# Performance work log

Hardware: AMD Instinct MI355X
Metric: run time of the kernel (lower is better)

The kernel has to match this reference:

```python
import jax, jax.numpy as jnp
import numpy as np

B, L, D = 32, 2048, 1024


def setup_inputs() -> dict:
    key = jax.random.key(0)
    ks = jax.random.split(key, 8)
    s = 1.0 / np.sqrt(D).astype(np.float32)  # torch nn.Linear init scale
    return {
        "decoder_hidden": jax.random.normal(ks[0], (B, 1, D), jnp.float32),
        "encoder_outputs": jax.random.normal(ks[1], (B, L, D), jnp.float32),
        "W_w": jax.random.uniform(ks[2], (D, D), jnp.float32, -s, s),
        "W_b": jax.random.uniform(ks[3], (D,), jnp.float32, -s, s),
        "U_w": jax.random.uniform(ks[4], (D, D), jnp.float32, -s, s),
        "U_b": jax.random.uniform(ks[5], (D,), jnp.float32, -s, s),
        "v_w": jax.random.uniform(ks[6], (1, D), jnp.float32, -s, s),
        "v_b": jax.random.uniform(ks[7], (1,), jnp.float32, -s, s),
    }


def reference(decoder_hidden, encoder_outputs, W_w, W_b, U_w, U_b, v_w, v_b):
    # torch Linear: y = x @ W.T + b
    q = decoder_hidden @ W_w.T + W_b            # [B, 1, D]
    k = encoder_outputs @ U_w.T + U_b           # [B, L, D]
    scores = jnp.tanh(q + k) @ v_w.T + v_b      # [B, L, 1]
    attn = jax.nn.softmax(scores[..., 0], axis=-1)[:, None, :]  # [B, 1, L]
    context = jnp.einsum("bql,bld->bqd", attn, encoder_outputs)  # [B, 1, D]
    return (context, attn)
```

## Files before the change

### kernel.cpp

```cpp
#include <hip/hip_runtime.h>
#include <hip/hip_bf16.h>
#include <stdint.h>

#define BB 32
#define LL 2048
#define DD 1024

typedef short short8  __attribute__((ext_vector_type(8)));
typedef float f32x4   __attribute__((ext_vector_type(4)));

__device__ __forceinline__ short f2bf(float f) {
    unsigned u = __float_as_uint(f);
    u += 0x7fffu + ((u >> 16) & 1u);
    return (short)(u >> 16);
}

__device__ __forceinline__ float bf2f(unsigned short s) {
    return __uint_as_float(((unsigned)s) << 16);
}

__device__ __forceinline__ float fast_tanh(float x) {
    float e = __expf(2.f * x);
    return 1.f - 2.f * __builtin_amdgcn_rcpf(e + 1.f);
}

__device__ __forceinline__ void async_cp16(const void* g, void* l) {
    __builtin_amdgcn_global_load_lds(
        (__attribute__((address_space(1))) void*)g,
        (__attribute__((address_space(3))) void*)l, 16, 0, 0);
}

__global__ void prep_kernel(const float* __restrict__ dh, const float* __restrict__ Ww,
                            const float* __restrict__ Wb, const float* __restrict__ Ub,
                            const float* __restrict__ Uw, const float* __restrict__ enc,
                            float* __restrict__ qbuf, short* __restrict__ Ubf,
                            short* __restrict__ encbf) {
    const int bid = blockIdx.x, t = threadIdx.x;
    if (bid >= 512) {
        const float* src = (bid < 1024) ? Uw : enc;
        short* dst = (bid < 1024) ? Ubf : encbf;
        int base = (bid < 1024) ? (bid - 512) : (bid - 1024);
        size_t idx = ((size_t)base * 256 + t) * 8;
        float4 a = *(const float4*)(src + idx);
        float4 c = *(const float4*)(src + idx + 4);
        short8 p;
        p[0] = f2bf(a.x); p[1] = f2bf(a.y); p[2] = f2bf(a.z); p[3] = f2bf(a.w);
        p[4] = f2bf(c.x); p[5] = f2bf(c.y); p[6] = f2bf(c.z); p[7] = f2bf(c.w);
        *(short8*)(dst + idx) = p;
        return;
    }
    int b  = bid >> 4;
    int d0 = (bid & 15) << 6;
    int w = t >> 6, lane = t & 63;
    __shared__ __align__(16) float hs[DD];
    *(float4*)&hs[t * 4] = *(const float4*)&dh[b * DD + t * 4];
    __syncthreads();
    float hr[16];
#pragma unroll
    for (int i = 0; i < 16; i++) hr[i] = hs[lane + 64 * i];
    for (int i = 0; i < 16; i++) {
        int d = d0 + w * 16 + i;
        const float* wr = Ww + (size_t)d * DD;
        float s = 0.f;
#pragma unroll
        for (int j = 0; j < 16; j++) s += wr[lane + 64 * j] * hr[j];
#pragma unroll
        for (int m = 1; m < 64; m <<= 1) s += __shfl_xor(s, m, 64);
        if (lane == 0) qbuf[b * DD + d] = s + Wb[d] + Ub[d];
    }
}

__global__ __launch_bounds__(256, 3) void gemm_scores_bf(
    const short* __restrict__ encbf, const short* __restrict__ Ubf,
    const float* __restrict__ qbuf, const float* __restrict__ vw,
    float* __restrict__ spart) {
    __shared__ __align__(16) short As[2][128 * 32];
    __shared__ __align__(16) short Bs[2][128 * 32];
    __shared__ float q_s[128], v_s[128], s_acc[2][128];

    const int t = threadIdx.x;
    const int lane = t & 63, w = t >> 6;
    const int l15 = lane & 15, quad = lane >> 4;
    const int wm = w >> 1, wn = w & 1;

    const int lin  = blockIdx.x + (blockIdx.y << 3);
    const int xcd  = lin & 7;
    const int slot = lin >> 3;
    const int nblk = slot & 7;
    const int mstripe = (xcd << 6) + (slot >> 3);
    const int n0 = nblk << 7;
    const int m0 = mstripe << 7;
    const int b  = m0 >> 11;

    if (t < 128) {
        q_s[t] = qbuf[(b << 10) + n0 + t];
        v_s[t] = vw[n0 + t];
    }

    f32x4 acc[4][4];
#pragma unroll
    for (int i = 0; i < 4; i++)
#pragma unroll
        for (int j = 0; j < 4; j++) acc[i][j] = (f32x4){0.f, 0.f, 0.f, 0.f};

    const int srow = lane >> 2, sseg = (lane & 3) << 3;
    const short* gA0 = encbf + (((size_t)(m0 + w * 32 + srow)) << 10) + sseg;
    const short* gB0 = Ubf   + (((size_t)(n0 + w * 32 + srow)) << 10) + sseg;
    const int lofs = w * 32 * 32;

    for (int k0 = 0; k0 < 1024; k0 += 64) {
        __syncthreads();
        async_cp16(gA0 + k0,                 &As[0][lofs]);
        async_cp16(gA0 + k0 + (16 << 10),    &As[0][lofs + 16 * 32]);
        async_cp16(gB0 + k0,                 &Bs[0][lofs]);
        async_cp16(gB0 + k0 + (16 << 10),    &Bs[0][lofs + 16 * 32]);
        async_cp16(gA0 + k0 + 32,            &As[1][lofs]);
        async_cp16(gA0 + k0 + 32 + (16 << 10), &As[1][lofs + 16 * 32]);
        async_cp16(gB0 + k0 + 32,            &Bs[1][lofs]);
        async_cp16(gB0 + k0 + 32 + (16 << 10), &Bs[1][lofs + 16 * 32]);
        __syncthreads();

#pragma unroll
        for (int h = 0; h < 2; h++) {
            short8 af[4], bfv[4];
#pragma unroll
            for (int mt = 0; mt < 4; mt++)
                af[mt] = *(const short8*)&As[h][(wm * 64 + mt * 16 + l15) * 32 + quad * 8];
#pragma unroll
            for (int nt = 0; nt < 4; nt++)
                bfv[nt] = *(const short8*)&Bs[h][(wn * 64 + nt * 16 + l15) * 32 + quad * 8];
#pragma unroll
            for (int mt = 0; mt < 4; mt++)
#pragma unroll
                for (int nt = 0; nt < 4; nt++)
                    acc[mt][nt] = __builtin_amdgcn_mfma_f32_16x16x32_bf16(
                        af[mt], bfv[nt], acc[mt][nt], 0, 0, 0);
        }
    }

    float qn[4], vn[4];
#pragma unroll
    for (int nt = 0; nt < 4; nt++) {
        qn[nt] = q_s[wn * 64 + nt * 16 + l15];
        vn[nt] = v_s[wn * 64 + nt * 16 + l15];
    }
#pragma unroll
    for (int mt = 0; mt < 4; mt++) {
#pragma unroll
        for (int r = 0; r < 4; r++) {
            float sum = 0.f;
#pragma unroll
            for (int nt = 0; nt < 4; nt++)
                sum += vn[nt] * fast_tanh(acc[mt][nt][r] + qn[nt]);
            sum += __shfl_xor(sum, 1, 64);
            sum += __shfl_xor(sum, 2, 64);
            sum += __shfl_xor(sum, 4, 64);
            sum += __shfl_xor(sum, 8, 64);
            if (l15 == 0)
                s_acc[wn][wm * 64 + mt * 16 + quad * 4 + r] = sum;
        }
    }
    __syncthreads();
    if (t < 128)
        spart[((size_t)nblk << 16) + m0 + t] = s_acc[0][t] + s_acc[1][t];
}

__global__ void ctx_softmax_bf(const float* __restrict__ sp, const short* __restrict__ encbf,
                               float* __restrict__ attn, float* __restrict__ ctx) {
    const int dchunk = blockIdx.x, b = blockIdx.y;
    const int t = threadIdx.x;
    const int w = t >> 6, lane = t & 63;
    __shared__ float at_s[2048];
    __shared__ float red[16][128];
    __shared__ float rr[8];

    float v[4];
#pragma unroll
    for (int i = 0; i < 4; i++) {
        int l = t + (i << 9);
        float s = 0.f;
#pragma unroll
        for (int p = 0; p < 8; p++) s += sp[(p << 16) + (b << 11) + l];
        v[i] = s;
    }
    float m = fmaxf(fmaxf(v[0], v[1]), fmaxf(v[2], v[3]));
#pragma unroll
    for (int s = 1; s < 64; s <<= 1) m = fmaxf(m, __shfl_xor(m, s, 64));
    if (lane == 0) rr[w] = m;
    __syncthreads();
    m = rr[0];
#pragma unroll
    for (int i = 1; i < 8; i++) m = fmaxf(m, rr[i]);
    float s = 0.f;
#pragma unroll
    for (int i = 0; i < 4; i++) { v[i] = __expf(v[i] - m); s += v[i]; }
#pragma unroll
    for (int k = 1; k < 64; k <<= 1) s += __shfl_xor(s, k, 64);
    __syncthreads();
    if (lane == 0) rr[w] = s;
#pragma unroll
    for (int i = 0; i < 4; i++) at_s[t + (i << 9)] = v[i];
    __syncthreads();
    s = 0.f;
#pragma unroll
    for (int i = 0; i < 8; i++) s += rr[i];
    float inv = 1.f / s;

    if (dchunk == 0) {
#pragma unroll
        for (int i = 0; i < 4; i++) attn[(b << 11) + t + (i << 9)] = v[i] * inv;
    }

    const int d4 = (t & 31) << 2;
    const int dl = t >> 5;
    const int d0 = dchunk << 7;
    const short* base = encbf + ((size_t)b << 21) + d0 + d4;
    float ax = 0.f, ay = 0.f, az = 0.f, aw = 0.f;
#pragma unroll 4
    for (int i = 0; i < 128; i++) {
        int l = (i << 4) + dl;
        float wg = at_s[l];
        ushort4 e = *(const ushort4*)(base + ((size_t)l << 10));
        ax += wg * bf2f(e.x); ay += wg * bf2f(e.y);
        az += wg * bf2f(e.z); aw += wg * bf2f(e.w);
    }
    red[dl][d4 + 0] = ax;
    red[dl][d4 + 1] = ay;
    red[dl][d4 + 2] = az;
    red[dl][d4 + 3] = aw;
    __syncthreads();
    if (t < 128) {
        float acc = 0.f;
#pragma unroll
        for (int j = 0; j < 16; j++) acc += red[j][t];
        ctx[(b << 10) + d0 + t] = acc * inv;
    }
}

__global__ void cvt_bf16_kernel(const float* __restrict__ src, short* __restrict__ dst) {
    int idx = (blockIdx.x * 256 + threadIdx.x) * 8;
    float4 a = *(const float4*)(src + idx);
    float4 c = *(const float4*)(src + idx + 4);
    short8 p;
    p[0] = f2bf(a.x); p[1] = f2bf(a.y); p[2] = f2bf(a.z); p[3] = f2bf(a.w);
    p[4] = f2bf(c.x); p[5] = f2bf(c.y); p[6] = f2bf(c.z); p[7] = f2bf(c.w);
    *(short8*)(dst + idx) = p;
}

__global__ void q_kernel(const float* __restrict__ dh, const float* __restrict__ Ww,
                         const float* __restrict__ Wb, const float* __restrict__ Ub,
                         float* __restrict__ qbuf) {
    int b  = blockIdx.x >> 4;
    int d0 = (blockIdx.x & 15) << 6;
    int t = threadIdx.x, w = t >> 6, lane = t & 63;
    __shared__ __align__(16) float hs[DD];
    *(float4*)&hs[t * 4] = *(const float4*)&dh[b * DD + t * 4];
    __syncthreads();
    float hr[16];
#pragma unroll
    for (int i = 0; i < 16; i++) hr[i] = hs[lane + 64 * i];
    for (int i = 0; i < 16; i++) {
        int d = d0 + w * 16 + i;
        const float* wr = Ww + (size_t)d * DD;
        float s = 0.f;
#pragma unroll
        for (int j = 0; j < 16; j++) s += wr[lane + 64 * j] * hr[j];
#pragma unroll
        for (int m = 1; m < 64; m <<= 1) s += __shfl_xor(s, m, 64);
        if (lane == 0) qbuf[b * DD + d] = s + Wb[d] + Ub[d];
    }
}

__global__ __launch_bounds__(256, 3) void gemm_scores_f32(
    const float* __restrict__ enc, const short* __restrict__ Ubf,
    const float* __restrict__ qbuf, const float* __restrict__ vw,
    float* __restrict__ scores) {
    __shared__ __align__(16) short As[128 * 32];
    __shared__ __align__(16) short Bs[128 * 32];
    __shared__ float q_s[128], v_s[128], s_acc[128];

    const int t = threadIdx.x;
    const int lane = t & 63, w = t >> 6;
    const int l15 = lane & 15, quad = lane >> 4;
    const int wm = w >> 1, wn = w & 1;
    const int n0 = blockIdx.x << 7;
    const int m0 = blockIdx.y << 7;
    const int b  = m0 >> 11;

    if (t < 128) {
        q_s[t] = qbuf[(b << 10) + n0 + t];
        v_s[t] = vw[n0 + t];
        s_acc[t] = 0.f;
    }

    f32x4 acc[4][4];
#pragma unroll
    for (int i = 0; i < 4; i++)
#pragma unroll
        for (int j = 0; j < 4; j++) acc[i][j] = (f32x4){0.f, 0.f, 0.f, 0.f};

    const int arow = t >> 1, ahalf = t & 1;
    const float* aptr = enc + (((size_t)(m0 + arow)) << 10) + (ahalf << 4);
    short* adst = As + arow * 32 + ahalf * 16;
    const int brow = t >> 2, bks = (t & 3) * 8;
    const short* bptr1 = Ubf + ((size_t)(n0 + brow)) * 1024 + bks;
    const short* bptr2 = bptr1 + (size_t)64 * 1024;
    short* bdst1 = Bs + brow * 32 + bks;
    short* bdst2 = bdst1 + 64 * 32;

    for (int k0 = 0; k0 < 1024; k0 += 32) {
        __syncthreads();
        float4 f0 = *(const float4*)(aptr + k0);
        float4 f1 = *(const float4*)(aptr + k0 + 4);
        float4 f2 = *(const float4*)(aptr + k0 + 8);
        float4 f3 = *(const float4*)(aptr + k0 + 12);
        short8 p0, p1;
        p0[0] = f2bf(f0.x); p0[1] = f2bf(f0.y); p0[2] = f2bf(f0.z); p0[3] = f2bf(f0.w);
        p0[4] = f2bf(f1.x); p0[5] = f2bf(f1.y); p0[6] = f2bf(f1.z); p0[7] = f2bf(f1.w);
        p1[0] = f2bf(f2.x); p1[1] = f2bf(f2.y); p1[2] = f2bf(f2.z); p1[3] = f2bf(f2.w);
        p1[4] = f2bf(f3.x); p1[5] = f2bf(f3.y); p1[6] = f2bf(f3.z); p1[7] = f2bf(f3.w);
        *(short8*)adst = p0;
        *(short8*)(adst + 8) = p1;
        *(short8*)bdst1 = *(const short8*)(bptr1 + k0);
        *(short8*)bdst2 = *(const short8*)(bptr2 + k0);
        __syncthreads();

        short8 af[4], bfv[4];
#pragma unroll
        for (int mt = 0; mt < 4; mt++)
            af[mt] = *(const short8*)&As[(wm * 64 + mt * 16 + l15) * 32 + quad * 8];
#pragma unroll
        for (int nt = 0; nt < 4; nt++)
            bfv[nt] = *(const short8*)&Bs[(wn * 64 + nt * 16 + l15) * 32 + quad * 8];
#pragma unroll
        for (int mt = 0; mt < 4; mt++)
#pragma unroll
            for (int nt = 0; nt < 4; nt++)
                acc[mt][nt] = __builtin_amdgcn_mfma_f32_16x16x32_bf16(
                    af[mt], bfv[nt], acc[mt][nt], 0, 0, 0);
    }

    float qn[4], vn[4];
#pragma unroll
    for (int nt = 0; nt < 4; nt++) {
        qn[nt] = q_s[wn * 64 + nt * 16 + l15];
        vn[nt] = v_s[wn * 64 + nt * 16 + l15];
    }
#pragma unroll
    for (int mt = 0; mt < 4; mt++) {
#pragma unroll
        for (int r = 0; r < 4; r++) {
            float sum = 0.f;
#pragma unroll
            for (int nt = 0; nt < 4; nt++)
                sum += vn[nt] * fast_tanh(acc[mt][nt][r] + qn[nt]);
            sum += __shfl_xor(sum, 1, 64);
            sum += __shfl_xor(sum, 2, 64);
            sum += __shfl_xor(sum, 4, 64);
            sum += __shfl_xor(sum, 8, 64);
            if (l15 == 0)
                atomicAdd(&s_acc[wm * 64 + mt * 16 + quad * 4 + r], sum);
        }
    }
    __syncthreads();
    if (t < 128) atomicAdd(&scores[m0 + t], s_acc[t]);
}

__global__ void softmax_kernel(const float* __restrict__ sp, float* __restrict__ attn) {
    int b = blockIdx.x, t = threadIdx.x;
    int w = t >> 6, lane = t & 63;
    __shared__ float rm[4], rs[4];
    float v[8];
#pragma unroll
    for (int i = 0; i < 8; i++) v[i] = sp[(b << 11) + t + (i << 8)];
    float m = v[0];
#pragma unroll
    for (int i = 1; i < 8; i++) m = fmaxf(m, v[i]);
#pragma unroll
    for (int s = 1; s < 64; s <<= 1) m = fmaxf(m, __shfl_xor(m, s, 64));
    if (lane == 0) rm[w] = m;
    __syncthreads();
    m = fmaxf(fmaxf(rm[0], rm[1]), fmaxf(rm[2], rm[3]));
    float s = 0.f;
#pragma unroll
    for (int i = 0; i < 8; i++) { v[i] = __expf(v[i] - m); s += v[i]; }
#pragma unroll
    for (int k = 1; k < 64; k <<= 1) s += __shfl_xor(s, k, 64);
    if (lane == 0) rs[w] = s;
    __syncthreads();
    s = rs[0] + rs[1] + rs[2] + rs[3];
    float inv = 1.f / s;
#pragma unroll
    for (int i = 0; i < 8; i++) attn[(b << 11) + t + (i << 8)] = v[i] * inv;
}

__global__ void context_f32(const float* __restrict__ enc, const float* __restrict__ attn,
                            float* __restrict__ ctx) {
    int dchunk = blockIdx.x, b = blockIdx.y;
    int t = threadIdx.x;
    __shared__ __align__(16) float at_s[2048];
    __shared__ float red[16][128];
    *(float4*)&at_s[t * 4] = *(const float4*)&attn[(b << 11) + t * 4];
    __syncthreads();
    int d4 = (t & 31) << 2;
    int dl = t >> 5;
    int d0 = dchunk << 7;
    const float* base = enc + ((size_t)b << 21) + d0 + d4;
    float ax = 0.f, ay = 0.f, az = 0.f, aw = 0.f;
#pragma unroll 4
    for (int i = 0; i < 128; i++) {
        int l = (i << 4) + dl;
        float wg = at_s[l];
        float4 e = *(const float4*)(base + ((size_t)l << 10));
        ax += wg * e.x; ay += wg * e.y; az += wg * e.z; aw += wg * e.w;
    }
    red[dl][d4 + 0] = ax;
    red[dl][d4 + 1] = ay;
    red[dl][d4 + 2] = az;
    red[dl][d4 + 3] = aw;
    __syncthreads();
    if (t < 128) {
        float s = 0.f;
#pragma unroll
        for (int j = 0; j < 16; j++) s += red[j][t];
        ctx[(b << 10) + d0 + t] = s;
    }
}

extern "C" void kernel_launch(void* const* d_in, const int* in_sizes, int n_in,
                              void* d_out, int out_size, void* d_ws, size_t ws_size,
                              hipStream_t stream) {
    const float* dh  = (const float*)d_in[0];
    const float* enc = (const float*)d_in[1];
    const float* Ww  = (const float*)d_in[2];
    const float* Wb  = (const float*)d_in[3];
    const float* Uw  = (const float*)d_in[4];
    const float* Ub  = (const float*)d_in[5];
    const float* vw  = (const float*)d_in[6];

    float* out  = (float*)d_out;
    float* attn = out + BB * DD;
    char*  ws   = (char*)d_ws;
    short* Ubf   = (short*)ws;
    float* qbuf  = (float*)(ws + (2 << 20));
    float* sbuf  = (float*)(ws + (2 << 20) + (1 << 17));
    short* encbf = (short*)(ws + (8 << 20));

    bool bigws = ws_size >= ((size_t)143 << 20);

    if (bigws) {
        prep_kernel<<<33792, 256, 0, stream>>>(dh, Ww, Wb, Ub, Uw, enc, qbuf, Ubf, encbf);
        gemm_scores_bf<<<dim3(8, 512), 256, 0, stream>>>(encbf, Ubf, qbuf, vw, sbuf);
        ctx_softmax_bf<<<dim3(8, BB), 512, 0, stream>>>(sbuf, encbf, attn, out);
    } else {
        hipMemsetAsync(sbuf, 0, (size_t)BB * LL * sizeof(float), stream);
        cvt_bf16_kernel<<<512, 256, 0, stream>>>(Uw, Ubf);
        q_kernel<<<512, 256, 0, stream>>>(dh, Ww, Wb, Ub, qbuf);
        gemm_scores_f32<<<dim3(8, 512), 256, 0, stream>>>(enc, Ubf, qbuf, vw, sbuf);
        softmax_kernel<<<BB, 256, 0, stream>>>(sbuf, attn);
        context_f32<<<dim3(8, BB), 512, 0, stream>>>(enc, attn, out);
    }
}
```

Baseline: 560.2 us.

## Fuse fp32-to-bf16 conversion of encoder outputs into the scores GEMM

Drops the separate encoder-conversion pass from the prep kernel. The scores GEMM now loads fp32 encoder rows, converts them to bf16 in registers and stores them into LDS. Blocks with nblk==0 also write the bf16 copy back to global memory for the context kernel. This avoids one full fp32 read and bf16 write of the 256MB encoder tensor. In exchange, every one of the 8 column blocks reads fp32 A (twice the bytes of bf16) through synchronous loads instead of async LDS copies, which can reduce overlap inside the GEMM.

```diff
diff --git a/kernel.cpp b/kernel.cpp
--- a/kernel.cpp
+++ b/kernel.cpp
@@ -30,23 +30,23 @@
         (__attribute__((address_space(3))) void*)l, 16, 0, 0);
 }
 
+__device__ __forceinline__ short8 pack8(float4 a, float4 b) {
+    short8 p;
+    p[0] = f2bf(a.x); p[1] = f2bf(a.y); p[2] = f2bf(a.z); p[3] = f2bf(a.w);
+    p[4] = f2bf(b.x); p[5] = f2bf(b.y); p[6] = f2bf(b.z); p[7] = f2bf(b.w);
+    return p;
+}
+
 __global__ void prep_kernel(const float* __restrict__ dh, const float* __restrict__ Ww,
                             const float* __restrict__ Wb, const float* __restrict__ Ub,
-                            const float* __restrict__ Uw, const float* __restrict__ enc,
-                            float* __restrict__ qbuf, short* __restrict__ Ubf,
-                            short* __restrict__ encbf) {
+                            const float* __restrict__ Uw,
+                            float* __restrict__ qbuf, short* __restrict__ Ubf) {
     const int bid = blockIdx.x, t = threadIdx.x;
     if (bid >= 512) {
-        const float* src = (bid < 1024) ? Uw : enc;
-        short* dst = (bid < 1024) ? Ubf : encbf;
-        int base = (bid < 1024) ? (bid - 512) : (bid - 1024);
-        size_t idx = ((size_t)base * 256 + t) * 8;
-        float4 a = *(const float4*)(src + idx);
-        float4 c = *(const float4*)(src + idx + 4);
-        short8 p;
-        p[0] = f2bf(a.x); p[1] = f2bf(a.y); p[2] = f2bf(a.z); p[3] = f2bf(a.w);
-        p[4] = f2bf(c.x); p[5] = f2bf(c.y); p[6] = f2bf(c.z); p[7] = f2bf(c.w);
-        *(short8*)(dst + idx) = p;
+        size_t idx = ((size_t)(bid - 512) * 256 + t) * 8;
+        float4 a = *(const float4*)(Uw + idx);
+        float4 c = *(const float4*)(Uw + idx + 4);
+        *(short8*)(Ubf + idx) = pack8(a, c);
         return;
     }
     int b  = bid >> 4;
@@ -70,10 +70,10 @@
     }
 }
 
-__global__ __launch_bounds__(256, 3) void gemm_scores_bf(
-    const short* __restrict__ encbf, const short* __restrict__ Ubf,
+__global__ __launch_bounds__(256, 3) void gemm_scores_fused(
+    const float* __restrict__ enc, const short* __restrict__ Ubf,
     const float* __restrict__ qbuf, const float* __restrict__ vw,
-    float* __restrict__ spart) {
+    float* __restrict__ spart, short* __restrict__ encbf) {
     __shared__ __align__(16) short As[2][128 * 32];
     __shared__ __align__(16) short Bs[2][128 * 32];
     __shared__ float q_s[128], v_s[128], s_acc[2][128];
@@ -104,21 +104,45 @@
         for (int j = 0; j < 4; j++) acc[i][j] = (f32x4){0.f, 0.f, 0.f, 0.f};
 
     const int srow = lane >> 2, sseg = (lane & 3) << 3;
-    const short* gA0 = encbf + (((size_t)(m0 + w * 32 + srow)) << 10) + sseg;
-    const short* gB0 = Ubf   + (((size_t)(n0 + w * 32 + srow)) << 10) + sseg;
+    const int rowA = m0 + w * 32 + srow;
+    const float* gA  = enc + ((size_t)rowA << 10) + sseg;
+    const short* gB0 = Ubf + (((size_t)(n0 + w * 32 + srow)) << 10) + sseg;
+    short* eW = encbf + ((size_t)rowA << 10) + sseg;
     const int lofs = w * 32 * 32;
+    short* la0 = &As[0][lofs + srow * 32 + sseg];
+    short* la1 = &As[1][lofs + srow * 32 + sseg];
+    const bool wb = (nblk == 0);
+    const int R16 = 16 << 10;
 
     for (int k0 = 0; k0 < 1024; k0 += 64) {
         __syncthreads();
-        async_cp16(gA0 + k0,                 &As[0][lofs]);
-        async_cp16(gA0 + k0 + (16 << 10),    &As[0][lofs + 16 * 32]);
-        async_cp16(gB0 + k0,                 &Bs[0][lofs]);
-        async_cp16(gB0 + k0 + (16 << 10),    &Bs[0][lofs + 16 * 32]);
-        async_cp16(gA0 + k0 + 32,            &As[1][lofs]);
-        async_cp16(gA0 + k0 + 32 + (16 << 10), &As[1][lofs + 16 * 32]);
-        async_cp16(gB0 + k0 + 32,            &Bs[1][lofs]);
-        async_cp16(gB0 + k0 + 32 + (16 << 10), &Bs[1][lofs + 16 * 32]);
+        async_cp16(gB0 + k0,              &Bs[0][lofs]);
+        async_cp16(gB0 + k0 + R16,        &Bs[0][lofs + 512]);
+        async_cp16(gB0 + k0 + 32,         &Bs[1][lofs]);
+        async_cp16(gB0 + k0 + 32 + R16,   &Bs[1][lofs + 512]);
+        float4 a0 = *(const float4*)(gA + k0);
+        float4 a1 = *(const float4*)(gA + k0 + 4);
+        float4 a2 = *(const float4*)(gA + k0 + R16);
+        float4 a3 = *(const float4*)(gA + k0 + R16 + 4);
+        float4 a4 = *(const float4*)(gA + k0 + 32);
+        float4 a5 = *(const float4*)(gA + k0 + 36);
+        float4 a6 = *(const float4*)(gA + k0 + R16 + 32);
+        float4 a7 = *(const float4*)(gA + k0 + R16 + 36);
+        short8 e0 = pack8(a0, a1);
+        short8 e1 = pack8(a2, a3);
+        short8 e2 = pack8(a4, a5);
+        short8 e3 = pack8(a6, a7);
+        *(short8*)la0 = e0;
+        *(short8*)(la0 + 512) = e1;
+        *(short8*)la1 = e2;
+        *(short8*)(la1 + 512) = e3;
         __syncthreads();
+        if (wb) {
+            *(short8*)(eW + k0)            = e0;
+            *(short8*)(eW + k0 + R16)      = e1;
+            *(short8*)(eW + k0 + 32)       = e2;
+            *(short8*)(eW + k0 + R16 + 32) = e3;
+        }
 
 #pragma unroll
         for (int h = 0; h < 2; h++) {
@@ -241,10 +265,7 @@
     int idx = (blockIdx.x * 256 + threadIdx.x) * 8;
     float4 a = *(const float4*)(src + idx);
     float4 c = *(const float4*)(src + idx + 4);
-    short8 p;
-    p[0] = f2bf(a.x); p[1] = f2bf(a.y); p[2] = f2bf(a.z); p[3] = f2bf(a.w);
-    p[4] = f2bf(c.x); p[5] = f2bf(c.y); p[6] = f2bf(c.z); p[7] = f2bf(c.w);
-    *(short8*)(dst + idx) = p;
+    *(short8*)(dst + idx) = pack8(a, c);
 }
 
 __global__ void q_kernel(const float* __restrict__ dh, const float* __restrict__ Ww,
@@ -314,13 +335,8 @@
         float4 f1 = *(const float4*)(aptr + k0 + 4);
         float4 f2 = *(const float4*)(aptr + k0 + 8);
         float4 f3 = *(const float4*)(aptr + k0 + 12);
-        short8 p0, p1;
-        p0[0] = f2bf(f0.x); p0[1] = f2bf(f0.y); p0[2] = f2bf(f0.z); p0[3] = f2bf(f0.w);
-        p0[4] = f2bf(f1.x); p0[5] = f2bf(f1.y); p0[6] = f2bf(f1.z); p0[7] = f2bf(f1.w);
-        p1[0] = f2bf(f2.x); p1[1] = f2bf(f2.y); p1[2] = f2bf(f2.z); p1[3] = f2bf(f2.w);
-        p1[4] = f2bf(f3.x); p1[5] = f2bf(f3.y); p1[6] = f2bf(f3.z); p1[7] = f2bf(f3.w);
-        *(short8*)adst = p0;
-        *(short8*)(adst + 8) = p1;
+        *(short8*)adst = pack8(f0, f1);
+        *(short8*)(adst + 8) = pack8(f2, f3);
         *(short8*)bdst1 = *(const short8*)(bptr1 + k0);
         *(short8*)bdst2 = *(const short8*)(bptr2 + k0);
         __syncthreads();
@@ -449,8 +465,8 @@
     bool bigws = ws_size >= ((size_t)143 << 20);
 
     if (bigws) {
-        prep_kernel<<<33792, 256, 0, stream>>>(dh, Ww, Wb, Ub, Uw, enc, qbuf, Ubf, encbf);
-        gemm_scores_bf<<<dim3(8, 512), 256, 0, stream>>>(encbf, Ubf, qbuf, vw, sbuf);
+        prep_kernel<<<1024, 256, 0, stream>>>(dh, Ww, Wb, Ub, Uw, qbuf, Ubf);
+        gemm_scores_fused<<<dim3(8, 512), 256, 0, stream>>>(enc, Ubf, qbuf, vw, sbuf, encbf);
         ctx_softmax_bf<<<dim3(8, BB), 512, 0, stream>>>(sbuf, encbf, attn, out);
     } else {
         hipMemsetAsync(sbuf, 0, (size_t)BB * LL * sizeof(float), stream);
```

Result: slower. 641.0 us (+14.4%).

## Split fused softmax-context kernel into softmax plus L-sliced context with atomics

Applied to the files above, without the earlier changes.

Replaces the fused softmax+context kernel (8x32 blocks, each recomputing the softmax) with a single softmax kernel per batch followed by a context kernel split over 8 L-slabs, giving 8x8x32 blocks that accumulate partial context sums into the output with atomicAdd. The aim is more parallelism for the bandwidth-bound bf16 encoder read and no redundant softmax recomputation. It costs an extra memset and launch, and float atomics make the summation order nondeterministic. The pack8 helper is a pure refactor.

```diff
diff --git a/kernel.cpp b/kernel.cpp
--- a/kernel.cpp
+++ b/kernel.cpp
@@ -28,6 +28,13 @@
     __builtin_amdgcn_global_load_lds(
         (__attribute__((address_space(1))) void*)g,
         (__attribute__((address_space(3))) void*)l, 16, 0, 0);
+}
+
+__device__ __forceinline__ short8 pack8(float4 a, float4 b) {
+    short8 p;
+    p[0] = f2bf(a.x); p[1] = f2bf(a.y); p[2] = f2bf(a.z); p[3] = f2bf(a.w);
+    p[4] = f2bf(b.x); p[5] = f2bf(b.y); p[6] = f2bf(b.z); p[7] = f2bf(b.w);
+    return p;
 }
 
 __global__ void prep_kernel(const float* __restrict__ dh, const float* __restrict__ Ww,
@@ -43,10 +50,7 @@
         size_t idx = ((size_t)base * 256 + t) * 8;
         float4 a = *(const float4*)(src + idx);
         float4 c = *(const float4*)(src + idx + 4);
-        short8 p;
-        p[0] = f2bf(a.x); p[1] = f2bf(a.y); p[2] = f2bf(a.z); p[3] = f2bf(a.w);
-        p[4] = f2bf(c.x); p[5] = f2bf(c.y); p[6] = f2bf(c.z); p[7] = f2bf(c.w);
-        *(short8*)(dst + idx) = p;
+        *(short8*)(dst + idx) = pack8(a, c);
         return;
     }
     int b  = bid >> 4;
@@ -165,60 +169,58 @@
         spart[((size_t)nblk << 16) + m0 + t] = s_acc[0][t] + s_acc[1][t];
 }
 
-__global__ void ctx_softmax_bf(const float* __restrict__ sp, const short* __restrict__ encbf,
-                               float* __restrict__ attn, float* __restrict__ ctx) {
-    const int dchunk = blockIdx.x, b = blockIdx.y;
-    const int t = threadIdx.x;
+__global__ void softmax8_kernel(const float* __restrict__ sp, float* __restrict__ attn) {
+    const int b = blockIdx.x, t = threadIdx.x;
     const int w = t >> 6, lane = t & 63;
-    __shared__ float at_s[2048];
-    __shared__ float red[16][128];
-    __shared__ float rr[8];
-
-    float v[4];
-#pragma unroll
-    for (int i = 0; i < 4; i++) {
-        int l = t + (i << 9);
+    __shared__ float rm[4], rs[4];
+    float v[8];
+#pragma unroll
+    for (int i = 0; i < 8; i++) {
+        int l = t + (i << 8);
         float s = 0.f;
 #pragma unroll
         for (int p = 0; p < 8; p++) s += sp[(p << 16) + (b << 11) + l];
         v[i] = s;
     }
-    float m = fmaxf(fmaxf(v[0], v[1]), fmaxf(v[2], v[3]));
+    float m = v[0];
+#pragma unroll
+    for (int i = 1; i < 8; i++) m = fmaxf(m, v[i]);
 #pragma unroll
     for (int s = 1; s < 64; s <<= 1) m = fmaxf(m, __shfl_xor(m, s, 64));
-    if (lane == 0) rr[w] = m;
-    __syncthreads();
-    m = rr[0];
-#pragma unroll
-    for (int i = 1; i < 8; i++) m = fmaxf(m, rr[i]);
+    if (lane == 0) rm[w] = m;
+    __syncthreads();
+    m = fmaxf(fmaxf(rm[0], rm[1]), fmaxf(rm[2], rm[3]));
     float s = 0.f;
 #pragma unroll
-    for (int i = 0; i < 4; i++) { v[i] = __expf(v[i] - m); s += v[i]; }
+    for (int i = 0; i < 8; i++) { v[i] = __expf(v[i] - m); s += v[i]; }
 #pragma unroll
     for (int k = 1; k < 64; k <<= 1) s += __shfl_xor(s, k, 64);
-    __syncthreads();
-    if (lane == 0) rr[w] = s;
-#pragma unroll
-    for (int i = 0; i < 4; i++) at_s[t + (i << 9)] = v[i];
-    __syncthreads();
-    s = 0.f;
-#pragma unroll
-    for (int i = 0; i < 8; i++) s += rr[i];
+    if (lane == 0) rs[w] = s;
+    __syncthreads();
+    s = rs[0] + rs[1] + rs[2] + rs[3];
     float inv = 1.f / s;
-
-    if (dchunk == 0) {
-#pragma unroll
-        for (int i = 0; i < 4; i++) attn[(b << 11) + t + (i << 9)] = v[i] * inv;
-    }
-
+#pragma unroll
+    for (int i = 0; i < 8; i++) attn[(b << 11) + t + (i << 8)] = v[i] * inv;
+}
+
+__global__ void ctx_part(const short* __restrict__ encbf, const float* __restrict__ attn,
+                         float* __restrict__ ctx) {
+    const int dchunk = blockIdx.x;
+    const int lslab  = blockIdx.y;
+    const int b      = blockIdx.z;
+    const int t = threadIdx.x;
+    __shared__ float at_s[256];
+    __shared__ float red[8][128];
+    at_s[t] = attn[(b << 11) + (lslab << 8) + t];
+    __syncthreads();
     const int d4 = (t & 31) << 2;
     const int dl = t >> 5;
     const int d0 = dchunk << 7;
-    const short* base = encbf + ((size_t)b << 21) + d0 + d4;
+    const short* base = encbf + ((size_t)b << 21) + ((size_t)lslab << 18) + d0 + d4;
     float ax = 0.f, ay = 0.f, az = 0.f, aw = 0.f;
-#pragma unroll 4
-    for (int i = 0; i < 128; i++) {
-        int l = (i << 4) + dl;
+#pragma unroll 8
+    for (int i = 0; i < 32; i++) {
+        int l = (i << 3) + dl;
         float wg = at_s[l];
         ushort4 e = *(const ushort4*)(base + ((size_t)l << 10));
         ax += wg * bf2f(e.x); ay += wg * bf2f(e.y);
@@ -230,10 +232,10 @@
     red[dl][d4 + 3] = aw;
     __syncthreads();
     if (t < 128) {
-        float acc = 0.f;
-#pragma unroll
-        for (int j = 0; j < 16; j++) acc += red[j][t];
-        ctx[(b << 10) + d0 + t] = acc * inv;
+        float s = 0.f;
+#pragma unroll
+        for (int j = 0; j < 8; j++) s += red[j][t];
+        atomicAdd(&ctx[(b << 10) + d0 + t], s);
     }
 }
 
@@ -241,10 +243,7 @@
     int idx = (blockIdx.x * 256 + threadIdx.x) * 8;
     float4 a = *(const float4*)(src + idx);
     float4 c = *(const float4*)(src + idx + 4);
-    short8 p;
-    p[0] = f2bf(a.x); p[1] = f2bf(a.y); p[2] = f2bf(a.z); p[3] = f2bf(a.w);
-    p[4] = f2bf(c.x); p[5] = f2bf(c.y); p[6] = f2bf(c.z); p[7] = f2bf(c.w);
-    *(short8*)(dst + idx) = p;
+    *(short8*)(dst + idx) = pack8(a, c);
 }
 
 __global__ void q_kernel(const float* __restrict__ dh, const float* __restrict__ Ww,
@@ -314,13 +313,8 @@
         float4 f1 = *(const float4*)(aptr + k0 + 4);
         float4 f2 = *(const float4*)(aptr + k0 + 8);
         float4 f3 = *(const float4*)(aptr + k0 + 12);
-        short8 p0, p1;
-        p0[0] = f2bf(f0.x); p0[1] = f2bf(f0.y); p0[2] = f2bf(f0.z); p0[3] = f2bf(f0.w);
-        p0[4] = f2bf(f1.x); p0[5] = f2bf(f1.y); p0[6] = f2bf(f1.z); p0[7] = f2bf(f1.w);
-        p1[0] = f2bf(f2.x); p1[1] = f2bf(f2.y); p1[2] = f2bf(f2.z); p1[3] = f2bf(f2.w);
-        p1[4] = f2bf(f3.x); p1[5] = f2bf(f3.y); p1[6] = f2bf(f3.z); p1[7] = f2bf(f3.w);
-        *(short8*)adst = p0;
-        *(short8*)(adst + 8) = p1;
+        *(short8*)adst = pack8(f0, f1);
+        *(short8*)(adst + 8) = pack8(f2, f3);
         *(short8*)bdst1 = *(const short8*)(bptr1 + k0);
         *(short8*)bdst2 = *(const short8*)(bptr2 + k0);
         __syncthreads();
@@ -449,9 +443,11 @@
     bool bigws = ws_size >= ((size_t)143 << 20);
 
     if (bigws) {
+        hipMemsetAsync(out, 0, (size_t)BB * DD * sizeof(float), stream);
         prep_kernel<<<33792, 256, 0, stream>>>(dh, Ww, Wb, Ub, Uw, enc, qbuf, Ubf, encbf);
         gemm_scores_bf<<<dim3(8, 512), 256, 0, stream>>>(encbf, Ubf, qbuf, vw, sbuf);
-        ctx_softmax_bf<<<dim3(8, BB), 512, 0, stream>>>(sbuf, encbf, attn, out);
+        softmax8_kernel<<<BB, 256, 0, stream>>>(sbuf, attn);
+        ctx_part<<<dim3(8, 8, BB), 256, 0, stream>>>(encbf, attn, out);
     } else {
         hipMemsetAsync(sbuf, 0, (size_t)BB * LL * sizeof(float), stream);
         cvt_bf16_kernel<<<512, 256, 0, stream>>>(Uw, Ubf);
```

Result: no change. 563.6 us (+0.6%).
